# Kernel optimization log

Measured on AMD Instinct MI355X. Metric: run time of the kernel, lower is better.

Reference implementation:

```python
import jax, jax.numpy as jnp
import numpy as np

B, T, D = 16, 4096, 512  # D = repeat * num_coeffs = 2 * 256

def setup_inputs() -> dict:
    key = jax.random.key(0)
    k1, k2, k3 = jax.random.split(key, 3)
    x = jax.random.normal(k1, (B, T, D), dtype=jnp.float32)
    # Stable diagonal complex transition: |A| < 1 so the recurrence doesn't blow up over T steps.
    A_real = jax.random.uniform(k2, (D,), dtype=jnp.float32, minval=-0.7, maxval=0.7)
    A_imag = jax.random.uniform(k3, (D,), dtype=jnp.float32, minval=-0.7, maxval=0.7)
    return {"x": x, "A_real": A_real, "A_imag": A_imag}

def reference(x, A_real, A_imag):
    # Diagonal complex linear recurrence (subsample_ratio=1 => every step updates):
    #   s_t = A * s_{t-1} + x_t,  with A = A_real + i*A_imag, s_0 = 0
    # Output per step: stack([Re(s_t), Im(s_t)], -1) -> [B, T, D, 2]
    xt = jnp.swapaxes(x, 0, 1)  # [T, B, D]

    def step(carry, x_t):
        sr, si = carry
        nr = sr * A_real - si * A_imag + x_t
        ni = A_imag * sr + A_real * si
        return (nr, ni), jnp.stack([nr, ni], axis=-1)

    init = (jnp.zeros((B, D), x.dtype), jnp.zeros((B, D), x.dtype))
    _, ys = jax.lax.scan(step, init, xt)  # ys: [T, B, D, 2]
    return jnp.swapaxes(ys, 0, 1)  # [B, T, D, 2]
```

## Files before the change

### kernel.cpp

```cpp
#include <hip/hip_runtime.h>


#define B_  16
#define T_  4096
#define D_  512
#define SEG 64
#define NS  (T_ / SEG)
#define BD  (B_ * D_)

typedef float v2f __attribute__((ext_vector_type(2)));
typedef float v4f __attribute__((ext_vector_type(4)));


__global__ __launch_bounds__(256) void seg_agg_kernel(
    const float* __restrict__ x,
    const float* __restrict__ Ar_g, const float* __restrict__ Ai_g,
    float2* __restrict__ buf) {
  int tid  = threadIdx.x;
  int lane = tid & 63;
  int g    = tid >> 6;
  int n    = blockIdx.x;
  int sq   = n & 15;
  int dt   = (n >> 4) & 3;
  int b    = n >> 6;
  int d    = dt * 128 + lane * 2;
  int seg  = sq * 4 + g;
  int t0   = seg * SEG;

  float2 Ar = *(const float2*)(Ar_g + d);
  float2 Ai = *(const float2*)(Ai_g + d);
  float s0r = 0.f, s0i = 0.f, s1r = 0.f, s1i = 0.f;
  const float2* xp = (const float2*)(x + ((size_t)(b * T_ + t0)) * D_ + d);
#pragma unroll 8
  for (int k = 0; k < SEG; ++k) {
    float2 xv = xp[(size_t)k * (D_ / 2)];
    float n0r = fmaf(s0r, Ar.x, fmaf(-s0i, Ai.x, xv.x));
    float n0i = fmaf(s0r, Ai.x, s0i * Ar.x);
    float n1r = fmaf(s1r, Ar.y, fmaf(-s1i, Ai.y, xv.y));
    float n1i = fmaf(s1r, Ai.y, s1i * Ar.y);
    s0r = n0r; s0i = n0i; s1r = n1r; s1i = n1i;
  }
  float4 agg = make_float4(s0r, s0i, s1r, s1i);
  *(float4*)(buf + (size_t)seg * BD + b * D_ + d) = agg;
}

__global__ __launch_bounds__(256) void apply_kernel(
    const float* __restrict__ x,
    const float* __restrict__ Ar_g, const float* __restrict__ Ai_g,
    const float2* __restrict__ buf,
    float4* __restrict__ out4) {
  int tid  = threadIdx.x;
  int lane = tid & 63;
  int g    = tid >> 6;
  int n    = blockIdx.x;
  int sq   = n & 15;
  int dt   = (n >> 4) & 3;
  int b    = n >> 6;
  int d    = dt * 128 + lane * 2;
  int seg  = sq * 4 + g;
  int t0   = seg * SEG;

  float2 Ar = *(const float2*)(Ar_g + d);
  float2 Ai = *(const float2*)(Ai_g + d);

  float p0r = Ar.x, p0i = Ai.x, p1r = Ar.y, p1i = Ai.y;
#pragma unroll
  for (int q = 0; q < 6; ++q) {
    float t0r = p0r * p0r - p0i * p0i; float t0i = 2.f * p0r * p0i;
    float t1r = p1r * p1r - p1i * p1i; float t1i = 2.f * p1r * p1i;
    p0r = t0r; p0i = t0i; p1r = t1r; p1i = t1i;
  }

  float S0r = 0.f, S0i = 0.f, S1r = 0.f, S1i = 0.f;
  const float* bbase = (const float*)(buf + b * D_ + d);
#pragma unroll 8
  for (int j = 0; j < seg; ++j) {
    float4 gv = *(const float4*)(bbase + (size_t)j * (BD * 2));
    float n0r = fmaf(p0r, S0r, fmaf(-p0i, S0i, gv.x));
    float n0i = fmaf(p0i, S0r, fmaf(p0r, S0i, gv.y));
    float n1r = fmaf(p1r, S1r, fmaf(-p1i, S1i, gv.z));
    float n1i = fmaf(p1i, S1r, fmaf(p1r, S1i, gv.w));
    S0r = n0r; S0i = n0i; S1r = n1r; S1i = n1i;
  }

  const v2f* xp = (const v2f*)(x + ((size_t)(b * T_ + t0)) * D_ + d);
  v4f* op = (v4f*)(out4 + (((size_t)(b * T_ + t0)) * D_ + d) / 2);
#pragma unroll 8
  for (int k = 0; k < SEG; ++k) {
    v2f xv = __builtin_nontemporal_load(xp + (size_t)k * (D_ / 2));
    float n0r = fmaf(S0r, Ar.x, fmaf(-S0i, Ai.x, xv.x));
    float n0i = fmaf(S0r, Ai.x, S0i * Ar.x);
    float n1r = fmaf(S1r, Ar.y, fmaf(-S1i, Ai.y, xv.y));
    float n1i = fmaf(S1r, Ai.y, S1i * Ar.y);
    S0r = n0r; S0i = n0i; S1r = n1r; S1i = n1i;
    v4f ov = {S0r, S0i, S1r, S1i};
    __builtin_nontemporal_store(ov, op + (size_t)k * (D_ / 2));
  }
}

extern "C" void kernel_launch(void* const* d_in, const int* in_sizes, int n_in,
                              void* d_out, int out_size, void* d_ws, size_t ws_size,
                              hipStream_t stream) {
  const float* x  = (const float*)d_in[0];
  const float* Ar = (const float*)d_in[1];
  const float* Ai = (const float*)d_in[2];
  float4* out = (float4*)d_out;
  float2* buf = (float2*)d_ws;

  seg_agg_kernel<<<dim3(1024), dim3(256), 0, stream>>>(x, Ar, Ai, buf);
  apply_kernel<<<dim3(1024), dim3(256), 0, stream>>>(x, Ar, Ai, buf, out);
}
```

Before: 378.1 us.

## Fuse segment aggregation and apply into one kernel with register-cached inputs

```diff
diff --git a/kernel.cpp b/kernel.cpp
--- a/kernel.cpp
+++ b/kernel.cpp
@@ -6,62 +6,44 @@
 #define D_  512
 #define SEG 64
 #define NS  (T_ / SEG)
-#define BD  (B_ * D_)
+#define NDP 16
 
 typedef float v2f __attribute__((ext_vector_type(2)));
 typedef float v4f __attribute__((ext_vector_type(4)));
 
-
-__global__ __launch_bounds__(256) void seg_agg_kernel(
+__global__ __launch_bounds__(1024, 4) void fused_scan_kernel(
     const float* __restrict__ x,
     const float* __restrict__ Ar_g, const float* __restrict__ Ai_g,
-    float2* __restrict__ buf) {
+    v4f* __restrict__ out4) {
   int tid  = threadIdx.x;
-  int lane = tid & 63;
-  int g    = tid >> 6;
+  int dp   = tid & (NDP - 1);
+  int seg  = tid >> 4;
   int n    = blockIdx.x;
-  int sq   = n & 15;
-  int dt   = (n >> 4) & 3;
-  int b    = n >> 6;
-  int d    = dt * 128 + lane * 2;
-  int seg  = sq * 4 + g;
+  int dblk = n & 15;
+  int b    = n >> 4;
+  int d    = dblk * (2 * NDP) + dp * 2;
   int t0   = seg * SEG;
+
+  __shared__ v4f agg[NS][NDP];
 
   float2 Ar = *(const float2*)(Ar_g + d);
   float2 Ai = *(const float2*)(Ai_g + d);
+
+  const v2f* xp = (const v2f*)(x + ((size_t)(b * T_ + t0)) * D_ + d);
+  float xa[SEG], xb[SEG];
   float s0r = 0.f, s0i = 0.f, s1r = 0.f, s1i = 0.f;
-  const float2* xp = (const float2*)(x + ((size_t)(b * T_ + t0)) * D_ + d);
-#pragma unroll 8
+#pragma unroll
   for (int k = 0; k < SEG; ++k) {
-    float2 xv = xp[(size_t)k * (D_ / 2)];
+    v2f xv = __builtin_nontemporal_load(xp + (size_t)k * (D_ / 2));
+    xa[k] = xv.x; xb[k] = xv.y;
     float n0r = fmaf(s0r, Ar.x, fmaf(-s0i, Ai.x, xv.x));
     float n0i = fmaf(s0r, Ai.x, s0i * Ar.x);
     float n1r = fmaf(s1r, Ar.y, fmaf(-s1i, Ai.y, xv.y));
     float n1i = fmaf(s1r, Ai.y, s1i * Ar.y);
     s0r = n0r; s0i = n0i; s1r = n1r; s1i = n1i;
   }
-  float4 agg = make_float4(s0r, s0i, s1r, s1i);
-  *(float4*)(buf + (size_t)seg * BD + b * D_ + d) = agg;
-}
-
-__global__ __launch_bounds__(256) void apply_kernel(
-    const float* __restrict__ x,
-    const float* __restrict__ Ar_g, const float* __restrict__ Ai_g,
-    const float2* __restrict__ buf,
-    float4* __restrict__ out4) {
-  int tid  = threadIdx.x;
-  int lane = tid & 63;
-  int g    = tid >> 6;
-  int n    = blockIdx.x;
-  int sq   = n & 15;
-  int dt   = (n >> 4) & 3;
-  int b    = n >> 6;
-  int d    = dt * 128 + lane * 2;
-  int seg  = sq * 4 + g;
-  int t0   = seg * SEG;
-
-  float2 Ar = *(const float2*)(Ar_g + d);
-  float2 Ai = *(const float2*)(Ai_g + d);
+  agg[seg][dp] = (v4f){s0r, s0i, s1r, s1i};
+  __syncthreads();
 
   float p0r = Ar.x, p0i = Ai.x, p1r = Ar.y, p1i = Ai.y;
 #pragma unroll
@@ -72,25 +54,21 @@
   }
 
   float S0r = 0.f, S0i = 0.f, S1r = 0.f, S1i = 0.f;
-  const float* bbase = (const float*)(buf + b * D_ + d);
-#pragma unroll 8
   for (int j = 0; j < seg; ++j) {
-    float4 gv = *(const float4*)(bbase + (size_t)j * (BD * 2));
-    float n0r = fmaf(p0r, S0r, fmaf(-p0i, S0i, gv.x));
-    float n0i = fmaf(p0i, S0r, fmaf(p0r, S0i, gv.y));
-    float n1r = fmaf(p1r, S1r, fmaf(-p1i, S1i, gv.z));
-    float n1i = fmaf(p1i, S1r, fmaf(p1r, S1i, gv.w));
+    v4f g = agg[j][dp];
+    float n0r = fmaf(p0r, S0r, fmaf(-p0i, S0i, g.x));
+    float n0i = fmaf(p0i, S0r, fmaf(p0r, S0i, g.y));
+    float n1r = fmaf(p1r, S1r, fmaf(-p1i, S1i, g.z));
+    float n1i = fmaf(p1i, S1r, fmaf(p1r, S1i, g.w));
     S0r = n0r; S0i = n0i; S1r = n1r; S1i = n1i;
   }
 
-  const v2f* xp = (const v2f*)(x + ((size_t)(b * T_ + t0)) * D_ + d);
-  v4f* op = (v4f*)(out4 + (((size_t)(b * T_ + t0)) * D_ + d) / 2);
-#pragma unroll 8
+  v4f* op = out4 + ((size_t)(b * T_ + t0)) * (D_ / 2) + (d >> 1);
+#pragma unroll
   for (int k = 0; k < SEG; ++k) {
-    v2f xv = __builtin_nontemporal_load(xp + (size_t)k * (D_ / 2));
-    float n0r = fmaf(S0r, Ar.x, fmaf(-S0i, Ai.x, xv.x));
+    float n0r = fmaf(S0r, Ar.x, fmaf(-S0i, Ai.x, xa[k]));
     float n0i = fmaf(S0r, Ai.x, S0i * Ar.x);
-    float n1r = fmaf(S1r, Ar.y, fmaf(-S1i, Ai.y, xv.y));
+    float n1r = fmaf(S1r, Ar.y, fmaf(-S1i, Ai.y, xb[k]));
     float n1i = fmaf(S1r, Ai.y, S1i * Ar.y);
     S0r = n0r; S0i = n0i; S1r = n1r; S1i = n1i;
     v4f ov = {S0r, S0i, S1r, S1i};
@@ -104,9 +82,7 @@
   const float* x  = (const float*)d_in[0];
   const float* Ar = (const float*)d_in[1];
   const float* Ai = (const float*)d_in[2];
-  float4* out = (float4*)d_out;
-  float2* buf = (float2*)d_ws;
+  v4f* out = (v4f*)d_out;
 
-  seg_agg_kernel<<<dim3(1024), dim3(256), 0, stream>>>(x, Ar, Ai, buf);
-  apply_kernel<<<dim3(1024), dim3(256), 0, stream>>>(x, Ar, Ai, buf, out);
+  fused_scan_kernel<<<dim3(256), dim3(1024), 0, stream>>>(x, Ar, Ai, out);
 }
```

New measurement: 370.9 us. No clear change (-1.9%).
